# Kernel optimization log

Measured on AMD Instinct MI355X. Metric: run time of the kernel, lower is better.

## Reference

```python
import math
import jax, jax.numpy as jnp
import numpy as np

NUM_HEADS = 16
NEG_INF = -1e30


def setup_inputs() -> dict:
    key = jax.random.key(0)
    k1, k2, k3, k4 = jax.random.split(key, 4)
    B, C, T = 4, 1024, 2048
    x = jax.random.normal(k1, (B, C, T), dtype=jnp.float32)
    mask = jax.random.randint(k2, (B, T), 0, 2, dtype=jnp.int32)
    # kernel-size-1 Conv1d with bias=False == matmul; torch init scale ~ 1/sqrt(fan_in)
    W_mem = jax.random.normal(k3, (2 * C, C), dtype=jnp.float32) / math.sqrt(C)
    W_q = jax.random.normal(k4, (C, C), dtype=jnp.float32) / math.sqrt(C)
    return {"x": x, "mask": mask, "W_mem": W_mem, "W_q": W_q}


def reference(x, mask, W_mem, W_q):
    B, C, T = x.shape
    nh = NUM_HEADS
    dh = C // nh
    # kernel-size-1 conv projections, output already transposed to [B, T, ch]
    memory = jnp.einsum('oc,bct->bto', W_mem, x)   # [B, T, 2C]
    query = jnp.einsum('oc,bct->bto', W_q, x)      # [B, T, C]
    Q = query.reshape(B, T, nh, dh).transpose(0, 2, 1, 3)           # [B, nh, T, dh]
    Km, Vm = jnp.split(memory, 2, axis=-1)
    K = Km.reshape(B, T, nh, dh).transpose(0, 2, 1, 3)              # [B, nh, T, dh]
    V = Vm.reshape(B, T, nh, dh).transpose(0, 2, 1, 3)              # [B, nh, T, dh]
    att = jnp.einsum('bhqd,bhkd->bhqk', Q, K) * (1.0 / math.sqrt(dh))
    m = mask.reshape(B, 1, 1, T).astype(att.dtype)
    logits = m * att + (1.0 - m) * NEG_INF  # masked_softmax convention
    weights = jax.nn.softmax(logits, axis=-1)
    # dropout is identity in eval mode
    out = jnp.einsum('bhqk,bhkd->bhqd', weights, V)                 # [B, nh, T, dh]
    return out.transpose(0, 2, 1, 3).reshape(B, T, C).transpose(0, 2, 1)  # [B, C, T]
```

## Files before the change

kernel.cpp:

```cpp
#include <hip/hip_runtime.h>

#define B_ 4
#define C_ 1024
#define T_ 2048
#define NH 16
#define DH 64
#define TC 3072

typedef __attribute__((ext_vector_type(8))) short short8;
typedef __attribute__((ext_vector_type(4))) short short4v;
typedef __attribute__((ext_vector_type(4))) float f32x4;
typedef __attribute__((ext_vector_type(16))) float f32x16;
typedef __attribute__((ext_vector_type(2))) unsigned int u32x2;
typedef __attribute__((ext_vector_type(4))) unsigned int u32x4;

#define S2Q 0.1803368801111204f

static __device__ __forceinline__ unsigned short f2bf(float f){
  unsigned int u = __builtin_bit_cast(unsigned int, f);
  u += 0x7fffu + ((u >> 16) & 1u);
  return (unsigned short)(u >> 16);
}

__global__ __launch_bounds__(256) void cast_w_kernel(const float* __restrict__ Wmem,
                                                     const float* __restrict__ Wq,
                                                     unsigned short* __restrict__ Wc){
  size_t base = ((size_t)blockIdx.x*256 + threadIdx.x)*4;
  float4 v;
  if (base < (size_t)2048*1024) v = *(const float4*)(Wmem + base);
  else                          v = *(const float4*)(Wq + (base - (size_t)2048*1024));
  short4v o;
  o.x = (short)f2bf(v.x); o.y = (short)f2bf(v.y);
  o.z = (short)f2bf(v.z); o.w = (short)f2bf(v.w);
  *(short4v*)(Wc + base) = o;
}

__global__ __launch_bounds__(256) void mask_bias_kernel(const int* __restrict__ mask,
                                                        float* __restrict__ fbias){
  int i = blockIdx.x*256 + threadIdx.x;
  fbias[i] = mask[i] ? 0.f : -1e30f;
}

__global__ __launch_bounds__(256) void transpose_x_kernel(const float* __restrict__ x,
                                                          unsigned short* __restrict__ xT){
  __shared__ float tile[32][33];
  int b = blockIdx.z;
  int c0 = blockIdx.y*32, t0 = blockIdx.x*32;
  int tx = threadIdx.x, ty = threadIdx.y;
  const float* xp = x + ((size_t)b*C_ + c0)*T_ + t0;
  #pragma unroll
  for (int i=0;i<4;i++) tile[ty+8*i][tx] = xp[(size_t)(ty+8*i)*T_ + tx];
  __syncthreads();
  unsigned short* op = xT + ((size_t)b*T_ + t0)*C_ + c0;
  int cp = tx & 15, tw = tx >> 4;
  #pragma unroll
  for (int i=0;i<2;i++){
    int trow = ty + 8*tw + 16*i;
    unsigned int pk = (unsigned int)f2bf(tile[2*cp][trow])
                    | ((unsigned int)f2bf(tile[2*cp+1][trow]) << 16);
    *(unsigned int*)(op + (size_t)trow*C_ + 2*cp) = pk;
  }
}

#define PBM 128
#define PBN 128
#define PBK 64

__global__ __launch_bounds__(256) void proj_gemm_kernel(const unsigned short* __restrict__ Wc,
    const unsigned short* __restrict__ xT,
    unsigned short* __restrict__ Kb, unsigned short* __restrict__ Vt,
    unsigned short* __restrict__ Qb){
  __shared__ unsigned short sA[PBM*PBK];
  __shared__ unsigned short sB[PBN*PBK];
  int b = blockIdx.y;
  int nbn = T_/PBN;
  int o0 = (int)(blockIdx.x / nbn)*PBM;
  int t0 = (int)(blockIdx.x % nbn)*PBN;
  int tid = threadIdx.x;
  int lane = tid & 63, wave = tid >> 6;
  int wr = wave >> 1, wc = wave & 1;
  f32x4 acc[4][4] = {};
  const unsigned short* Abase = Wc + (size_t)o0*C_;
  const unsigned short* Bbase = xT + ((size_t)b*T_ + t0)*C_;
  auto ldsA = (__attribute__((address_space(3))) char*)sA;
  auto ldsB = (__attribute__((address_space(3))) char*)sB;
  for (int k0=0; k0<C_; k0+=PBK){
    #pragma unroll
    for (int i=0;i<4;i++){
      int L  = wave*4096 + i*1024;
      int Ll = L + lane*16;
      int row = Ll >> 7;
      int jb  = Ll & 127;
      const char* srcA = (const char*)(Abase + (size_t)row*C_ + k0) + jb;
      const char* srcB = (const char*)(Bbase + (size_t)row*C_ + k0) + jb;
      __builtin_amdgcn_global_load_lds((const __attribute__((address_space(1))) void*)srcA,
                                       (__attribute__((address_space(3))) void*)(ldsA + L), 16, 0, 0);
      __builtin_amdgcn_global_load_lds((const __attribute__((address_space(1))) void*)srcB,
                                       (__attribute__((address_space(3))) void*)(ldsB + L), 16, 0, 0);
    }
    __syncthreads();
    #pragma unroll
    for (int ks=0; ks<2; ks++){
      short8 af[4], bfr[4];
      #pragma unroll
      for (int m=0;m<4;m++){
        int row = wr*64 + m*16 + (lane & 15);
        af[m] = *(const short8*)((const char*)sA + row*128 + ks*64 + ((lane>>4)*16));
      }
      #pragma unroll
      for (int n=0;n<4;n++){
        int row = wc*64 + n*16 + (lane & 15);
        bfr[n] = *(const short8*)((const char*)sB + row*128 + ks*64 + ((lane>>4)*16));
      }
      #pragma unroll
      for (int m=0;m<4;m++){
        #pragma unroll
        for (int n=0;n<4;n++)
          acc[m][n] = __builtin_amdgcn_mfma_f32_16x16x32_bf16(af[m], bfr[n], acc[m][n], 0, 0, 0);
      }
    }
    __syncthreads();
  }
  int rowbase = o0 + wr*64;
  #pragma unroll
  for (int m=0;m<4;m++){
    int o = rowbase + m*16 + ((lane>>4)*4);
    #pragma unroll
    for (int n=0;n<4;n++){
      int t = t0 + wc*64 + n*16 + (lane & 15);
      f32x4 v = acc[m][n];
      if (o < C_){
        int h = o >> 6, d = o & 63;
        unsigned short* p = Kb + (((size_t)(b*NH + h)*T_ + t)*DH + d);
        short4v s; s.x=(short)f2bf(v.x); s.y=(short)f2bf(v.y);
        s.z=(short)f2bf(v.z); s.w=(short)f2bf(v.w);
        *(short4v*)p = s;
      } else if (o < 2*C_){
        int oo = o - C_;
        int h = oo >> 6, d = oo & 63;
        unsigned short* p = Vt + (((size_t)(b*NH + h)*DH + d)*T_ + t);
        p[0]    = f2bf(v.x);
        p[T_]   = f2bf(v.y);
        p[2*T_] = f2bf(v.z);
        p[3*T_] = f2bf(v.w);
      } else {
        int oo = o - 2*C_;
        int h = oo >> 6, d = oo & 63;
        unsigned short* p = Qb + (((size_t)(b*NH + h)*T_ + t)*DH + d);
        short4v s; s.x=(short)f2bf(v.x*S2Q); s.y=(short)f2bf(v.y*S2Q);
        s.z=(short)f2bf(v.z*S2Q); s.w=(short)f2bf(v.w*S2Q);
        *(short4v*)p = s;
      }
    }
  }
}

#define KB_ 64

#define GLL(SRC, SHBUF, LOFF) \
  __builtin_amdgcn_global_load_lds((const __attribute__((address_space(1))) void*)(SRC), \
      (__attribute__((address_space(3))) void*)((__attribute__((address_space(3))) char*)(SHBUF) + (LOFF)), 16, 0, 0)

#define TILE(CBUF, POFF, DOSTAGE) do {                                                 \
  if (DOSTAGE) {                                                                       \
    GLL(srcK0, &sK[(CBUF)^1][0], L0);                                                  \
    GLL(srcK1, &sK[(CBUF)^1][0], L0 + 1024);                                           \
    GLL(srcV0, &sV[(CBUF)^1][0], L0);                                                  \
    GLL(srcV1, &sV[(CBUF)^1][0], L0 + 1024);                                           \
    srcK0 += 8192; srcK1 += 8192; srcV0 += 128; srcV1 += 128;                          \
  }                                                                                    \
  f32x4 bbA[4], bbB[4];                                                                \
  _Pragma("unroll")                                                                    \
  for (int m=0;m<4;m++){                                                               \
    bbA[m] = *(const f32x4*)(bptr + (POFF) + m*8);                                     \
    bbB[m] = *(const f32x4*)(bptr + (POFF) + 32 + m*8);                                \
  }                                                                                    \
  const char* sKb = (const char*)&sK[CBUF][0] + l31*128;                               \
  const char* sVb = (const char*)&sV[CBUF][0] + l31*128;                               \
  f32x16 s0 = {}, s1 = {};                                                             \
  __builtin_amdgcn_s_setprio(1);                                                       \
  _Pragma("unroll")                                                                    \
  for (int kc=0;kc<4;kc++){                                                            \
    int co = (((kc<<1)|h) ^ rsw) << 4;                                                 \
    short8 kf0 = *(const short8*)(sKb + co);                                           \
    short8 kf1 = *(const short8*)(sKb + 4096 + co);                                    \
    s0 = __builtin_amdgcn_mfma_f32_32x32x16_bf16(kf0, qf[kc], s0, 0,0,0);              \
    s1 = __builtin_amdgcn_mfma_f32_32x32x16_bf16(kf1, qf[kc], s1, 0,0,0);              \
  }                                                                                    \
  __builtin_amdgcn_s_setprio(0);                                                       \
  float p[32];                                                                         \
  _Pragma("unroll")                                                                    \
  for (int m=0;m<4;m++){                                                               \
    _Pragma("unroll")                                                                  \
    for (int s=0;s<4;s++){                                                             \
      p[m*4+s]    = s0[m*4+s] + bbA[m][s];                                             \
      p[16+m*4+s] = s1[m*4+s] + bbB[m][s];                                             \
    }                                                                                  \
  }                                                                                    \
  float pmax = p[0];                                                                   \
  _Pragma("unroll")                                                                    \
  for (int j=1;j<32;j++) pmax = fmaxf(pmax, p[j]);                                     \
  if (!__all(pmax - mrun <= 8.0f)){                                                    \
    float pm = fmaxf(pmax, __shfl_xor(pmax, 32));                                      \
    float mnew = fmaxf(mrun, pm);                                                      \
    float alpha = __builtin_amdgcn_exp2f(mrun - mnew);                                 \
    mrun = mnew; lpart *= alpha;                                                       \
    _Pragma("unroll")                                                                  \
    for (int r=0;r<16;r++){                                                            \
      float ar = __shfl(alpha, (r&3) + 8*(r>>2) + 4*h);                                \
      acco0[r] *= ar; acco1[r] *= ar;                                                  \
    }                                                                                  \
  }                                                                                    \
  float ps_ = 0.f;                                                                     \
  _Pragma("unroll")                                                                    \
  for (int j=0;j<32;j++){ p[j] = __builtin_amdgcn_exp2f(p[j] - mrun); ps_ += p[j]; }   \
  lpart += ps_;                                                                        \
  unsigned int Wp[2][4][2];                                                            \
  _Pragma("unroll")                                                                    \
  for (int m=0;m<4;m++){                                                               \
    asm volatile("v_cvt_pk_bf16_f32 %0, %1, %2" : "=v"(Wp[0][m][0]) : "v"(p[4*m]),    "v"(p[4*m+1]));  \
    asm volatile("v_cvt_pk_bf16_f32 %0, %1, %2" : "=v"(Wp[0][m][1]) : "v"(p[4*m+2]),  "v"(p[4*m+3]));  \
    asm volatile("v_cvt_pk_bf16_f32 %0, %1, %2" : "=v"(Wp[1][m][0]) : "v"(p[16+4*m]), "v"(p[16+4*m+1]));\
    asm volatile("v_cvt_pk_bf16_f32 %0, %1, %2" : "=v"(Wp[1][m][1]) : "v"(p[16+4*m+2]),"v"(p[16+4*m+3]));\
  }                                                                                    \
  __builtin_amdgcn_s_setprio(1);                                                       \
  _Pragma("unroll")                                                                    \
  for (int kb=0;kb<2;kb++){                                                            \
    _Pragma("unroll")                                                                  \
    for (int e=0;e<2;e++){                                                             \
      u32x2 x0 = __builtin_amdgcn_permlane32_swap(Wp[kb][2*e][0], Wp[kb][2*e+1][0], 0, 0); \
      u32x2 x1 = __builtin_amdgcn_permlane32_swap(Wp[kb][2*e][1], Wp[kb][2*e+1][1], 0, 0); \
      u32x4 pw; pw.x = x0.x; pw.y = x1.x; pw.z = x0.y; pw.w = x1.y;                    \
      short8 pf = __builtin_bit_cast(short8, pw);                                      \
      int vo = (((((kb<<1)|e)<<1)|h) ^ rsw) << 4;                                      \
      short8 vf0 = *(const short8*)(sVb + vo);                                         \
      short8 vf1 = *(const short8*)(sVb + 4096 + vo);                                  \
      acco0 = __builtin_amdgcn_mfma_f32_32x32x16_bf16(pf, vf0, acco0, 0,0,0);          \
      acco1 = __builtin_amdgcn_mfma_f32_32x32x16_bf16(pf, vf1, acco1, 0,0,0);          \
    }                                                                                  \
  }                                                                                    \
  __builtin_amdgcn_s_setprio(0);                                                       \
  __syncthreads();                                                                     \
} while(0)

__global__ __launch_bounds__(256) void attn_kernel(const unsigned short* __restrict__ Qb,
    const unsigned short* __restrict__ Kb, const unsigned short* __restrict__ Vt,
    const float* __restrict__ fbias, float* __restrict__ out){
  __shared__ unsigned short sK[2][KB_*DH];
  __shared__ unsigned short sV[2][KB_*DH];
  const int Lid = blockIdx.x;
  const int xcd = Lid & 7, jj = Lid >> 3;
  const int bh = ((jj & 7) << 3) | xcd;
  const int qblk = jj >> 3;
  const int b = bh >> 4;
  const int tid = threadIdx.x, lane = tid & 63, wave = tid >> 6;
  const int l31 = lane & 31, h = lane >> 5;
  const int rsw = l31 & 7;
  const unsigned short* Kbase = Kb + (size_t)bh*T_*DH;
  const unsigned short* Vbase = Vt + (size_t)bh*DH*T_;
  const float* bptr = fbias + (size_t)b*T_ + 4*h;
  const int qrow = qblk*128 + wave*32 + l31;
  const unsigned short* Qp = Qb + ((size_t)bh*T_ + qrow)*DH + h*8;
  short8 qf[4];
  #pragma unroll
  for (int kc=0;kc<4;kc++) qf[kc] = *(const short8*)(Qp + kc*16);
  f32x16 acco0 = {}, acco1 = {};
  float mrun = -1e30f, lpart = 0.f;
  const int L0  = wave*2048;
  const int Ll0 = L0 + lane*16, Ll1 = Ll0 + 1024;
  const int row0 = Ll0 >> 7, row1 = Ll1 >> 7;
  const int cg0 = ((Ll0 >> 4) & 7) ^ (row0 & 7);
  const int cg1 = ((Ll1 >> 4) & 7) ^ (row1 & 7);
  const char* srcK0 = (const char*)Kbase + row0*128 + cg0*16;
  const char* srcK1 = (const char*)Kbase + row1*128 + cg1*16;
  const char* srcV0 = (const char*)Vbase + (size_t)row0*(T_*2) + cg0*16;
  const char* srcV1 = (const char*)Vbase + (size_t)row1*(T_*2) + cg1*16;

  GLL(srcK0, &sK[0][0], L0);
  GLL(srcK1, &sK[0][0], L0 + 1024);
  GLL(srcV0, &sV[0][0], L0);
  GLL(srcV1, &sV[0][0], L0 + 1024);
  srcK0 += 8192; srcK1 += 8192; srcV0 += 128; srcV1 += 128;
  __syncthreads();

  for (int kt2 = 0; kt2 < T_/KB_/2 - 1; kt2++){
    TILE(0,  0, true);
    TILE(1, 64, true);
    bptr += 128;
  }
  TILE(0,  0, true);
  TILE(1, 64, false);

  lpart += __shfl_xor(lpart, 32);
  float inv = 1.0f / lpart;
  const int head = bh & 15;
  const int qbase = qblk*128 + wave*32;
  #pragma unroll
  for (int m=0;m<4;m++){
    float rv[4];
    #pragma unroll
    for (int s=0;s<4;s++) rv[s] = __shfl(inv, 8*m + 4*h + s);
    int t = qbase + 8*m + 4*h;
    float4 v0, v1;
    v0.x = acco0[4*m+0]*rv[0]; v0.y = acco0[4*m+1]*rv[1];
    v0.z = acco0[4*m+2]*rv[2]; v0.w = acco0[4*m+3]*rv[3];
    v1.x = acco1[4*m+0]*rv[0]; v1.y = acco1[4*m+1]*rv[1];
    v1.z = acco1[4*m+2]*rv[2]; v1.w = acco1[4*m+3]*rv[3];
    size_t off0 = ((size_t)b*C_ + head*64 + l31)*T_ + t;
    size_t off1 = ((size_t)b*C_ + head*64 + 32 + l31)*T_ + t;
    *(float4*)(out + off0) = v0;
    *(float4*)(out + off1) = v1;
  }
}

extern "C" void kernel_launch(void* const* d_in, const int* in_sizes, int n_in,
                              void* d_out, int out_size, void* d_ws, size_t ws_size,
                              hipStream_t stream) {
  const float* x    = (const float*)d_in[0];
  const int*   mask = (const int*)d_in[1];
  const float* Wmem = (const float*)d_in[2];
  const float* Wq   = (const float*)d_in[3];
  float* out = (float*)d_out;

  unsigned short* ws = (unsigned short*)d_ws;
  unsigned short* xT = ws;
  unsigned short* Wc = xT + (size_t)B_*T_*C_;
  unsigned short* Qb = Wc + (size_t)TC*C_;
  unsigned short* Kb = Qb + (size_t)B_*NH*T_*DH;
  unsigned short* Vt = Kb + (size_t)B_*NH*T_*DH;
  float* fbias = (float*)(Vt + (size_t)B_*NH*T_*DH);

  cast_w_kernel<<<dim3(TC*C_/1024), dim3(256), 0, stream>>>(Wmem, Wq, Wc);
  mask_bias_kernel<<<dim3(B_*T_/256), dim3(256), 0, stream>>>(mask, fbias);
  transpose_x_kernel<<<dim3(T_/32, C_/32, B_), dim3(32,8), 0, stream>>>(x, xT);
  proj_gemm_kernel<<<dim3((TC/PBM)*(T_/PBN), B_), dim3(256), 0, stream>>>(Wc, xT, Kb, Vt, Qb);
  attn_kernel<<<dim3((T_/128)*(B_*NH)), dim3(256), 0, stream>>>(Qb, Kb, Vt, fbias, out);
}
```

Baseline: 206.6 us.

## Use 512-thread attention blocks covering 256 queries with shared K/V tiles

The attention kernel now launches 8 waves per block, each block handling 256 query rows, so every K/V tile staged in shared memory is reused by twice as many waves and each thread issues half as many global-to-LDS loads. The grid is halved to match. The running-max reduction is rewritten as a tree of three-input max operations, and the bias loads are moved ahead of the async staging. The cost is fewer blocks in the grid (512) and larger blocks that may limit occupancy or scheduling flexibility per CU.

```diff
diff --git a/kernel.cpp b/kernel.cpp
--- a/kernel.cpp
+++ b/kernel.cpp
@@ -161,19 +161,19 @@
   __builtin_amdgcn_global_load_lds((const __attribute__((address_space(1))) void*)(SRC), \
       (__attribute__((address_space(3))) void*)((__attribute__((address_space(3))) char*)(SHBUF) + (LOFF)), 16, 0, 0)
 
+#define MAX3(a,b,c) fmaxf(fmaxf((a),(b)),(c))
+
 #define TILE(CBUF, POFF, DOSTAGE) do {                                                 \
-  if (DOSTAGE) {                                                                       \
-    GLL(srcK0, &sK[(CBUF)^1][0], L0);                                                  \
-    GLL(srcK1, &sK[(CBUF)^1][0], L0 + 1024);                                           \
-    GLL(srcV0, &sV[(CBUF)^1][0], L0);                                                  \
-    GLL(srcV1, &sV[(CBUF)^1][0], L0 + 1024);                                           \
-    srcK0 += 8192; srcK1 += 8192; srcV0 += 128; srcV1 += 128;                          \
-  }                                                                                    \
   f32x4 bbA[4], bbB[4];                                                                \
   _Pragma("unroll")                                                                    \
   for (int m=0;m<4;m++){                                                               \
     bbA[m] = *(const f32x4*)(bptr + (POFF) + m*8);                                     \
     bbB[m] = *(const f32x4*)(bptr + (POFF) + 32 + m*8);                                \
+  }                                                                                    \
+  if (DOSTAGE) {                                                                       \
+    GLL(srcK, &sK[(CBUF)^1][0], L0);                                                   \
+    GLL(srcV, &sV[(CBUF)^1][0], L0);                                                   \
+    srcK += 8192; srcV += 128;                                                         \
   }                                                                                    \
   const char* sKb = (const char*)&sK[CBUF][0] + l31*128;                               \
   const char* sVb = (const char*)&sV[CBUF][0] + l31*128;                               \
@@ -197,9 +197,14 @@
       p[16+m*4+s] = s1[m*4+s] + bbB[m][s];                                             \
     }                                                                                  \
   }                                                                                    \
-  float pmax = p[0];                                                                   \
-  _Pragma("unroll")                                                                    \
-  for (int j=1;j<32;j++) pmax = fmaxf(pmax, p[j]);                                     \
+  float t0_ = MAX3(p[0],p[1],p[2]),  t1_ = MAX3(p[3],p[4],p[5]);                       \
+  float t2_ = MAX3(p[6],p[7],p[8]),  t3_ = MAX3(p[9],p[10],p[11]);                     \
+  float t4_ = MAX3(p[12],p[13],p[14]), t5_ = MAX3(p[15],p[16],p[17]);                  \
+  float t6_ = MAX3(p[18],p[19],p[20]), t7_ = MAX3(p[21],p[22],p[23]);                  \
+  float t8_ = MAX3(p[24],p[25],p[26]), t9_ = MAX3(p[27],p[28],p[29]);                  \
+  float u0_ = MAX3(t0_,t1_,t2_), u1_ = MAX3(t3_,t4_,t5_);                              \
+  float u2_ = MAX3(t6_,t7_,t8_), u3_ = MAX3(t9_,p[30],p[31]);                          \
+  float pmax = MAX3(MAX3(u0_,u1_,u2_), u3_, -1e30f);                                   \
   if (!__all(pmax - mrun <= 8.0f)){                                                    \
     float pm = fmaxf(pmax, __shfl_xor(pmax, 32));                                      \
     float mnew = fmaxf(mrun, pm);                                                      \
@@ -243,7 +248,7 @@
   __syncthreads();                                                                     \
 } while(0)
 
-__global__ __launch_bounds__(256) void attn_kernel(const unsigned short* __restrict__ Qb,
+__global__ __launch_bounds__(512) void attn_kernel(const unsigned short* __restrict__ Qb,
     const unsigned short* __restrict__ Kb, const unsigned short* __restrict__ Vt,
     const float* __restrict__ fbias, float* __restrict__ out){
   __shared__ unsigned short sK[2][KB_*DH];
@@ -259,28 +264,23 @@
   const unsigned short* Kbase = Kb + (size_t)bh*T_*DH;
   const unsigned short* Vbase = Vt + (size_t)bh*DH*T_;
   const float* bptr = fbias + (size_t)b*T_ + 4*h;
-  const int qrow = qblk*128 + wave*32 + l31;
+  const int qrow = qblk*256 + wave*32 + l31;
   const unsigned short* Qp = Qb + ((size_t)bh*T_ + qrow)*DH + h*8;
   short8 qf[4];
   #pragma unroll
   for (int kc=0;kc<4;kc++) qf[kc] = *(const short8*)(Qp + kc*16);
   f32x16 acco0 = {}, acco1 = {};
   float mrun = -1e30f, lpart = 0.f;
-  const int L0  = wave*2048;
-  const int Ll0 = L0 + lane*16, Ll1 = Ll0 + 1024;
-  const int row0 = Ll0 >> 7, row1 = Ll1 >> 7;
+  const int L0  = wave*1024;
+  const int Ll0 = L0 + lane*16;
+  const int row0 = Ll0 >> 7;
   const int cg0 = ((Ll0 >> 4) & 7) ^ (row0 & 7);
-  const int cg1 = ((Ll1 >> 4) & 7) ^ (row1 & 7);
-  const char* srcK0 = (const char*)Kbase + row0*128 + cg0*16;
-  const char* srcK1 = (const char*)Kbase + row1*128 + cg1*16;
-  const char* srcV0 = (const char*)Vbase + (size_t)row0*(T_*2) + cg0*16;
-  const char* srcV1 = (const char*)Vbase + (size_t)row1*(T_*2) + cg1*16;
-
-  GLL(srcK0, &sK[0][0], L0);
-  GLL(srcK1, &sK[0][0], L0 + 1024);
-  GLL(srcV0, &sV[0][0], L0);
-  GLL(srcV1, &sV[0][0], L0 + 1024);
-  srcK0 += 8192; srcK1 += 8192; srcV0 += 128; srcV1 += 128;
+  const char* srcK = (const char*)Kbase + row0*128 + cg0*16;
+  const char* srcV = (const char*)Vbase + (size_t)row0*(T_*2) + cg0*16;
+
+  GLL(srcK, &sK[0][0], L0);
+  GLL(srcV, &sV[0][0], L0);
+  srcK += 8192; srcV += 128;
   __syncthreads();
 
   for (int kt2 = 0; kt2 < T_/KB_/2 - 1; kt2++){
@@ -294,7 +294,7 @@
   lpart += __shfl_xor(lpart, 32);
   float inv = 1.0f / lpart;
   const int head = bh & 15;
-  const int qbase = qblk*128 + wave*32;
+  const int qbase = qblk*256 + wave*32;
   #pragma unroll
   for (int m=0;m<4;m++){
     float rv[4];
@@ -334,5 +334,5 @@
   mask_bias_kernel<<<dim3(B_*T_/256), dim3(256), 0, stream>>>(mask, fbias);
   transpose_x_kernel<<<dim3(T_/32, C_/32, B_), dim3(32,8), 0, stream>>>(x, xT);
   proj_gemm_kernel<<<dim3((TC/PBM)*(T_/PBN), B_), dim3(256), 0, stream>>>(Wc, xT, Kb, Vt, Qb);
-  attn_kernel<<<dim3((T_/128)*(B_*NH)), dim3(256), 0, stream>>>(Qb, Kb, Vt, fbias, out);
-}
+  attn_kernel<<<dim3((T_/256)*(B_*NH)), dim3(512), 0, stream>>>(Qb, Kb, Vt, fbias, out);
+}
```

Result: slower. 214.8 us (+3.9%).

## Fold mask bias into MFMA accumulator init and hand-schedule waitcnt barriers

Applied to the files above, without the earlier changes.

Loads the per-key bias directly into the QK^T MFMA accumulators, so the separate add pass and the p[] copy go away and exp works in place. The row max now uses a max3 tree. __syncthreads is replaced by explicit s_waitcnt vmcnt plus s_barrier at the start of each tile and sched_barriers, and s_setprio is removed, so the global-to-LDS prefetch can stay in flight across the tile boundary. The hard-coded vmcnt counts depend on the exact number of outstanding loads, and any mismatch risks reading LDS data before it arrives.

```diff
diff --git a/kernel.cpp b/kernel.cpp
--- a/kernel.cpp
+++ b/kernel.cpp
@@ -161,24 +161,30 @@
   __builtin_amdgcn_global_load_lds((const __attribute__((address_space(1))) void*)(SRC), \
       (__attribute__((address_space(3))) void*)((__attribute__((address_space(3))) char*)(SHBUF) + (LOFF)), 16, 0, 0)
 
+#define MAX3(a,b,c) fmaxf(fmaxf((a),(b)),(c))
+
 #define TILE(CBUF, POFF, DOSTAGE) do {                                                 \
+  union { f32x4 q[4]; f32x16 v; } cb0, cb1;                                            \
+  _Pragma("unroll")                                                                    \
+  for (int m=0;m<4;m++){                                                               \
+    cb0.q[m] = *(const f32x4*)(bptr + (POFF) + m*8);                                   \
+    cb1.q[m] = *(const f32x4*)(bptr + (POFF) + 32 + m*8);                              \
+  }                                                                                    \
   if (DOSTAGE) {                                                                       \
     GLL(srcK0, &sK[(CBUF)^1][0], L0);                                                  \
     GLL(srcK1, &sK[(CBUF)^1][0], L0 + 1024);                                           \
     GLL(srcV0, &sV[(CBUF)^1][0], L0);                                                  \
     GLL(srcV1, &sV[(CBUF)^1][0], L0 + 1024);                                           \
     srcK0 += 8192; srcK1 += 8192; srcV0 += 128; srcV1 += 128;                          \
-  }                                                                                    \
-  f32x4 bbA[4], bbB[4];                                                                \
-  _Pragma("unroll")                                                                    \
-  for (int m=0;m<4;m++){                                                               \
-    bbA[m] = *(const f32x4*)(bptr + (POFF) + m*8);                                     \
-    bbB[m] = *(const f32x4*)(bptr + (POFF) + 32 + m*8);                                \
-  }                                                                                    \
+    asm volatile("s_waitcnt vmcnt(12)" ::: "memory");                                  \
+  } else {                                                                             \
+    asm volatile("s_waitcnt vmcnt(8)" ::: "memory");                                   \
+  }                                                                                    \
+  __builtin_amdgcn_s_barrier();                                                        \
+  __builtin_amdgcn_sched_barrier(0);                                                   \
   const char* sKb = (const char*)&sK[CBUF][0] + l31*128;                               \
   const char* sVb = (const char*)&sV[CBUF][0] + l31*128;                               \
-  f32x16 s0 = {}, s1 = {};                                                             \
-  __builtin_amdgcn_s_setprio(1);                                                       \
+  f32x16 s0 = cb0.v, s1 = cb1.v;                                                       \
   _Pragma("unroll")                                                                    \
   for (int kc=0;kc<4;kc++){                                                            \
     int co = (((kc<<1)|h) ^ rsw) << 4;                                                 \
@@ -187,19 +193,14 @@
     s0 = __builtin_amdgcn_mfma_f32_32x32x16_bf16(kf0, qf[kc], s0, 0,0,0);              \
     s1 = __builtin_amdgcn_mfma_f32_32x32x16_bf16(kf1, qf[kc], s1, 0,0,0);              \
   }                                                                                    \
-  __builtin_amdgcn_s_setprio(0);                                                       \
-  float p[32];                                                                         \
-  _Pragma("unroll")                                                                    \
-  for (int m=0;m<4;m++){                                                               \
-    _Pragma("unroll")                                                                  \
-    for (int s=0;s<4;s++){                                                             \
-      p[m*4+s]    = s0[m*4+s] + bbA[m][s];                                             \
-      p[16+m*4+s] = s1[m*4+s] + bbB[m][s];                                             \
-    }                                                                                  \
-  }                                                                                    \
-  float pmax = p[0];                                                                   \
-  _Pragma("unroll")                                                                    \
-  for (int j=1;j<32;j++) pmax = fmaxf(pmax, p[j]);                                     \
+  float t0_ = MAX3(s0[0],s0[1],s0[2]),   t1_ = MAX3(s0[3],s0[4],s0[5]);                \
+  float t2_ = MAX3(s0[6],s0[7],s0[8]),   t3_ = MAX3(s0[9],s0[10],s0[11]);              \
+  float t4_ = MAX3(s0[12],s0[13],s0[14]), t5_ = MAX3(s0[15],s1[0],s1[1]);              \
+  float t6_ = MAX3(s1[2],s1[3],s1[4]),   t7_ = MAX3(s1[5],s1[6],s1[7]);                \
+  float t8_ = MAX3(s1[8],s1[9],s1[10]),  t9_ = MAX3(s1[11],s1[12],s1[13]);             \
+  float u0_ = MAX3(t0_,t1_,t2_), u1_ = MAX3(t3_,t4_,t5_);                              \
+  float u2_ = MAX3(t6_,t7_,t8_), u3_ = MAX3(t9_,s1[14],s1[15]);                        \
+  float pmax = MAX3(MAX3(u0_,u1_,u2_), u3_, -1e30f);                                   \
   if (!__all(pmax - mrun <= 8.0f)){                                                    \
     float pm = fmaxf(pmax, __shfl_xor(pmax, 32));                                      \
     float mnew = fmaxf(mrun, pm);                                                      \
@@ -213,17 +214,19 @@
   }                                                                                    \
   float ps_ = 0.f;                                                                     \
   _Pragma("unroll")                                                                    \
-  for (int j=0;j<32;j++){ p[j] = __builtin_amdgcn_exp2f(p[j] - mrun); ps_ += p[j]; }   \
+  for (int j=0;j<16;j++){                                                              \
+    s0[j] = __builtin_amdgcn_exp2f(s0[j] - mrun); ps_ += s0[j];                        \
+    s1[j] = __builtin_amdgcn_exp2f(s1[j] - mrun); ps_ += s1[j];                        \
+  }                                                                                    \
   lpart += ps_;                                                                        \
   unsigned int Wp[2][4][2];                                                            \
   _Pragma("unroll")                                                                    \
   for (int m=0;m<4;m++){                                                               \
-    asm volatile("v_cvt_pk_bf16_f32 %0, %1, %2" : "=v"(Wp[0][m][0]) : "v"(p[4*m]),    "v"(p[4*m+1]));  \
-    asm volatile("v_cvt_pk_bf16_f32 %0, %1, %2" : "=v"(Wp[0][m][1]) : "v"(p[4*m+2]),  "v"(p[4*m+3]));  \
-    asm volatile("v_cvt_pk_bf16_f32 %0, %1, %2" : "=v"(Wp[1][m][0]) : "v"(p[16+4*m]), "v"(p[16+4*m+1]));\
-    asm volatile("v_cvt_pk_bf16_f32 %0, %1, %2" : "=v"(Wp[1][m][1]) : "v"(p[16+4*m+2]),"v"(p[16+4*m+3]));\
-  }                                                                                    \
-  __builtin_amdgcn_s_setprio(1);                                                       \
+    asm volatile("v_cvt_pk_bf16_f32 %0, %1, %2" : "=v"(Wp[0][m][0]) : "v"(s0[4*m]),   "v"(s0[4*m+1]));  \
+    asm volatile("v_cvt_pk_bf16_f32 %0, %1, %2" : "=v"(Wp[0][m][1]) : "v"(s0[4*m+2]), "v"(s0[4*m+3]));  \
+    asm volatile("v_cvt_pk_bf16_f32 %0, %1, %2" : "=v"(Wp[1][m][0]) : "v"(s1[4*m]),   "v"(s1[4*m+1]));  \
+    asm volatile("v_cvt_pk_bf16_f32 %0, %1, %2" : "=v"(Wp[1][m][1]) : "v"(s1[4*m+2]), "v"(s1[4*m+3]));  \
+  }                                                                                    \
   _Pragma("unroll")                                                                    \
   for (int kb=0;kb<2;kb++){                                                            \
     _Pragma("unroll")                                                                  \
@@ -239,8 +242,8 @@
       acco1 = __builtin_amdgcn_mfma_f32_32x32x16_bf16(pf, vf1, acco1, 0,0,0);          \
     }                                                                                  \
   }                                                                                    \
-  __builtin_amdgcn_s_setprio(0);                                                       \
-  __syncthreads();                                                                     \
+  __builtin_amdgcn_sched_barrier(0);                                                   \
+  __builtin_amdgcn_s_barrier();                                                        \
 } while(0)
 
 __global__ __launch_bounds__(256) void attn_kernel(const unsigned short* __restrict__ Qb,
```

New measurement: 200.9 us. -2.8%, faster.
